# Kernel tuning notes

Measured on AMD Instinct MI355X. Metric: run time of the kernel, lower is better.

The kernel has to match this reference:

```python
import jax, jax.numpy as jnp
import numpy as np

EPS_COMBINE = float(np.finfo(float).eps)  # combined[combined == 0] = np.finfo(float).eps
LOSS_COEF = 0.01


def cv_squared(v):
    # torch .var() is unbiased -> ddof=1
    return jnp.var(v, ddof=1) / (jnp.mean(v) ** 2 + 1e-10)


def setup_inputs() -> dict:
    key = jax.random.key(0)
    k1, k2, k3, k4 = jax.random.split(key, 4)
    B, D, E, C = 4096, 1024, 8, 4096
    x = jax.random.normal(k1, (B, D), jnp.float32)
    # small scale so exp(expert_out) in combine() stays finite
    w_gate = jax.random.normal(k2, (D, E), jnp.float32) * 0.02
    w_exp = jax.random.normal(k3, (E, D, C), jnp.float32) * 0.02
    b_exp = jax.random.normal(k4, (E, C), jnp.float32) * 0.02
    return {"x": x, "w_gate": w_gate, "w_exp": w_exp, "b_exp": b_exp, "k": 4}


def reference(x, w_gate, w_exp, b_exp, k):
    B, D = x.shape
    E = w_gate.shape[1]
    # --- noisy_top_k_gating with noisy_gating=False ---
    logits = x @ w_gate                                   # [B, E]
    top_logits, top_idx = jax.lax.top_k(logits, min(k + 1, E))
    topk_logits = top_logits[:, :k]
    topk_idx = top_idx[:, :k]
    topk_gates = jax.nn.softmax(topk_logits, axis=1)      # softmax over top-k only
    gates = jnp.zeros((B, E), x.dtype).at[jnp.arange(B)[:, None], topk_idx].set(topk_gates)
    importance = gates.sum(0)
    load = (gates > 0).sum(0).astype(jnp.float32)         # _gates_to_load
    loss = (cv_squared(importance) + cv_squared(load)) * LOSS_COEF
    # --- dispatch + per-expert forward + weighted combine ---
    # Experts with gate==0 contribute exactly 0 to the combine, so the dense
    # einsum over all experts computes the same math as SparseDispatcher.
    expert_out = jnp.einsum('bd,edc->bec', x, w_exp) + b_exp   # [B, E, C]
    combined = jnp.einsum('bec,be->bc', jnp.exp(expert_out), gates)  # weighted scatter-combine
    combined = jnp.where(combined == 0, EPS_COMBINE, combined)
    y = jnp.log(combined)
    return y, loss
```

## Files before the change

### kernel.cpp

```cpp
#include <hip/hip_runtime.h>
#include <stdint.h>

#define B_ROWS 4096
#define D_DIM  1024
#define E_NUM  8
#define C_DIM  4096
#define LOSS_COEF 0.01f
#define EPS_COMBINE 2.220446049250313e-16f

typedef float  f32x4  __attribute__((ext_vector_type(4)));
typedef __bf16 bf16x8 __attribute__((ext_vector_type(8)));

static __device__ __forceinline__ unsigned short f2bf(float f) {
    unsigned int u = __float_as_uint(f);
    u += 0x7fffu + ((u >> 16) & 1u);
    return (unsigned short)(u >> 16);
}

static __device__ __forceinline__ void async16(const void* g, void* l) {
    __builtin_amdgcn_global_load_lds(
        (const __attribute__((address_space(1))) unsigned int*)g,
        (__attribute__((address_space(3))) unsigned int*)l, 16, 0, 0);
}

__global__ void zero_stats_kernel(float* __restrict__ stats) {
    if (threadIdx.x < 16) stats[threadIdx.x] = 0.0f;
}

__global__ __launch_bounds__(256) void transpose_wexp_kernel(
    const float* __restrict__ wexp, unsigned short* __restrict__ wT) {
    __shared__ float T[64][68];
    __shared__ unsigned short W[64][72];
    const int e  = blockIdx.z;
    const int k0 = blockIdx.y * 64;
    const int c0 = blockIdx.x * 64;
    const int t  = threadIdx.x;
    const float* src = wexp + ((size_t)e * D_DIM + k0) * C_DIM + c0;
    #pragma unroll
    for (int i = 0; i < 4; ++i) {
        int kr = i * 16 + (t >> 4);
        int cg = (t & 15) * 4;
        *(float4*)&T[kr][cg] = *(const float4*)(src + (size_t)kr * C_DIM + cg);
    }
    __syncthreads();
    {
        const int c  = t & 63;
        const int kq = (t >> 6) * 16;
        unsigned short h[16];
        #pragma unroll
        for (int j = 0; j < 16; ++j) h[j] = f2bf(T[kq + j][c]);
        *(uint4*)&W[c][kq]     = ((const uint4*)h)[0];
        *(uint4*)&W[c][kq + 8] = ((const uint4*)h)[1];
    }
    __syncthreads();
    unsigned short* dstb = wT + (size_t)e * C_DIM * D_DIM;
    #pragma unroll
    for (int r = 0; r < 2; ++r) {
        int i  = r * 256 + t;
        int c3 = i >> 3;
        int k8 = (i & 7) * 8;
        *(uint4*)(dstb + (size_t)(c0 + c3) * D_DIM + k0 + k8) = *(const uint4*)&W[c3][k8];
    }
}

__global__ __launch_bounds__(256) void gating_kernel(
    const float* __restrict__ x,
    const float* __restrict__ wg,
    unsigned short* __restrict__ xb,
    float* __restrict__ gates,
    float* __restrict__ stats) {
    __shared__ float simp[E_NUM], sload[E_NUM];
    const int tid = threadIdx.x;
    if (tid < E_NUM) { simp[tid] = 0.0f; sload[tid] = 0.0f; }
    __syncthreads();
    const int lane = tid & 63;
    const int wid  = tid >> 6;
    const int row  = blockIdx.x * 4 + wid;

    float acc[8] = {0.f,0.f,0.f,0.f,0.f,0.f,0.f,0.f};
    #pragma unroll
    for (int i = 0; i < 4; ++i) {
        int d = i * 256 + lane * 4;
        float4 xv = *(const float4*)(x + (size_t)row * D_DIM + d);
        unsigned short hh[4] = { f2bf(xv.x), f2bf(xv.y), f2bf(xv.z), f2bf(xv.w) };
        *(uint2*)(xb + (size_t)row * D_DIM + d) = *(const uint2*)hh;
        float xa[4] = { xv.x, xv.y, xv.z, xv.w };
        #pragma unroll
        for (int j = 0; j < 4; ++j) {
            const float4* wp = (const float4*)(wg + (size_t)(d + j) * 8);
            float4 w0 = wp[0], w1 = wp[1];
            acc[0] += xa[j] * w0.x; acc[1] += xa[j] * w0.y;
            acc[2] += xa[j] * w0.z; acc[3] += xa[j] * w0.w;
            acc[4] += xa[j] * w1.x; acc[5] += xa[j] * w1.y;
            acc[6] += xa[j] * w1.z; acc[7] += xa[j] * w1.w;
        }
    }
    #pragma unroll
    for (int off = 32; off > 0; off >>= 1)
        #pragma unroll
        for (int e = 0; e < 8; ++e)
            acc[e] += __shfl_xor(acc[e], off, 64);
    if (lane == 0) {
        float val[4]; int idx[4]; unsigned used = 0;
        #pragma unroll
        for (int j = 0; j < 4; ++j) {
            float best = -1e30f; int bi = 0;
            for (int ee = 0; ee < 8; ++ee)
                if (!(used & (1u << ee)) && acc[ee] > best) { best = acc[ee]; bi = ee; }
            used |= 1u << bi; val[j] = best; idx[j] = bi;
        }
        float mx = val[0], sum = 0.f, gv[4];
        #pragma unroll
        for (int j = 0; j < 4; ++j) { gv[j] = __expf(val[j] - mx); sum += gv[j]; }
        float inv = 1.0f / sum;
        float gout[8] = {0.f,0.f,0.f,0.f,0.f,0.f,0.f,0.f};
        #pragma unroll
        for (int j = 0; j < 4; ++j) gout[idx[j]] = gv[j] * inv;
        #pragma unroll
        for (int e = 0; e < 8; ++e) gates[(size_t)row * 8 + e] = gout[e];
        #pragma unroll
        for (int j = 0; j < 4; ++j) {
            atomicAdd(&simp[idx[j]], gv[j] * inv);
            atomicAdd(&sload[idx[j]], 1.0f);
        }
    }
    __syncthreads();
    if (tid < E_NUM) {
        atomicAdd(&stats[tid],          simp[tid]);
        atomicAdd(&stats[E_NUM + tid],  sload[tid]);
    }
}

__global__ void loss_kernel(const float* __restrict__ stats, float* __restrict__ out_loss) {
    if (threadIdx.x == 0) {
        float mi = 0.f, ml = 0.f;
        for (int e = 0; e < 8; ++e) { mi += stats[e]; ml += stats[8 + e]; }
        mi *= 0.125f; ml *= 0.125f;
        float vi = 0.f, vl = 0.f;
        for (int e = 0; e < 8; ++e) {
            float a = stats[e] - mi;     vi += a * a;
            float b = stats[8 + e] - ml; vl += b * b;
        }
        vi *= (1.0f / 7.0f); vl *= (1.0f / 7.0f);
        out_loss[0] = (vi / (mi * mi + 1e-10f) + vl / (ml * ml + 1e-10f)) * LOSS_COEF;
    }
}

__global__ __launch_bounds__(256, 3) void moe_main_kernel(
    const unsigned short* __restrict__ xb,
    const unsigned short* __restrict__ wT,
    const float* __restrict__ bexp,
    const float* __restrict__ gates,
    float* __restrict__ out)
{
    __shared__ unsigned short As[128 * 32];
    __shared__ unsigned short Bs[2 * 64 * 32];
    __shared__ float gs[128 * 9];
    __shared__ float bs[8 * 64];

    const int tid  = threadIdx.x;
    const int lane = tid & 63;
    const int wid  = tid >> 6;
    const int wm   = wid >> 1;
    const int wn   = wid & 1;
    const int q    = lane >> 4;
    const int ln   = lane & 15;
    const int row0 = blockIdx.x * 128;
    const int col0 = blockIdx.y * 64;

    #pragma unroll
    for (int i = 0; i < 4; ++i) {
        int idx = i * 256 + tid;
        gs[(idx >> 3) * 9 + (idx & 7)] = gates[(size_t)row0 * 8 + idx];
    }
    {
        int e = tid >> 5, c = tid & 31;
        bs[e * 64 + c]      = bexp[(size_t)e * C_DIM + col0 + c];
        bs[e * 64 + c + 32] = bexp[(size_t)e * C_DIM + col0 + c + 32];
    }

    const f32x4 vzero = {0.f, 0.f, 0.f, 0.f};
    f32x4 comb[4][2];
    #pragma unroll
    for (int i = 0; i < 4; ++i)
        #pragma unroll
        for (int j = 0; j < 2; ++j) comb[i][j] = vzero;

    const int rS = tid >> 2;
    const int qg = (tid & 3) ^ (rS & 3);
    const unsigned short* gA  = xb + (size_t)(row0 + rS) * D_DIM + qg * 8;
    const unsigned short* gBb = wT + (size_t)(col0 + rS) * D_DIM + qg * 8;
    char* ldsA = (char*)As + wid * 1024;
    char* ldsB = (char*)Bs + wid * 1024;

    const int fq = ((q ^ (ln & 3)) << 3);

    for (int eg = 0; eg < 4; ++eg) {
        f32x4 acc[4][2][2];
        #pragma unroll
        for (int i = 0; i < 4; ++i)
            #pragma unroll
            for (int j = 0; j < 2; ++j)
                #pragma unroll
                for (int e = 0; e < 2; ++e) acc[i][j][e] = vzero;

        const unsigned short* gB0 = gBb + (size_t)(2 * eg)     * C_DIM * D_DIM;
        const unsigned short* gB1 = gBb + (size_t)(2 * eg + 1) * C_DIM * D_DIM;

        for (int kt = 0; kt < D_DIM / 32; ++kt) {
            const int ko = kt * 32;
            async16(gA + ko,               ldsA);
            async16(gA + ko + 64 * D_DIM,  ldsA + 4096);
            async16(gB0 + ko,              ldsB);
            async16(gB1 + ko,              ldsB + 4096);

            __syncthreads();

            bf16x8 af[4], bfr[2][2];
            #pragma unroll
            for (int fm = 0; fm < 4; ++fm)
                af[fm] = *(const bf16x8*)(As + (wm * 64 + fm * 16 + ln) * 32 + fq);
            #pragma unroll
            for (int fn = 0; fn < 2; ++fn)
                #pragma unroll
                for (int e = 0; e < 2; ++e)
                    bfr[fn][e] = *(const bf16x8*)(Bs + e * 2048 +
                                    (wn * 32 + fn * 16 + ln) * 32 + fq);
            #pragma unroll
            for (int fm = 0; fm < 4; ++fm)
                #pragma unroll
                for (int fn = 0; fn < 2; ++fn)
                    #pragma unroll
                    for (int e = 0; e < 2; ++e)
                        acc[fm][fn][e] = __builtin_amdgcn_mfma_f32_16x16x32_bf16(
                            af[fm], bfr[fn][e], acc[fm][fn][e], 0, 0, 0);

            __syncthreads();
        }

        #pragma unroll
        for (int e = 0; e < 2; ++e) {
            int eG = eg * 2 + e;
            #pragma unroll
            for (int fn = 0; fn < 2; ++fn) {
                float bval = bs[eG * 64 + wn * 32 + fn * 16 + ln];
                #pragma unroll
                for (int fm = 0; fm < 4; ++fm)
                    #pragma unroll
                    for (int r = 0; r < 4; ++r) {
                        float g = gs[(wm * 64 + fm * 16 + q * 4 + r) * 9 + eG];
                        comb[fm][fn][r] += g * __expf(acc[fm][fn][e][r] + bval);
                    }
            }
        }
    }

    #pragma unroll
    for (int fm = 0; fm < 4; ++fm)
        #pragma unroll
        for (int fn = 0; fn < 2; ++fn)
            #pragma unroll
            for (int r = 0; r < 4; ++r) {
                int row = row0 + wm * 64 + fm * 16 + q * 4 + r;
                int col = col0 + wn * 32 + fn * 16 + ln;
                float c = comb[fm][fn][r];
                c = (c == 0.0f) ? EPS_COMBINE : c;
                out[(size_t)row * C_DIM + col] = __logf(c);
            }
}

extern "C" void kernel_launch(void* const* d_in, const int* in_sizes, int n_in,
                              void* d_out, int out_size, void* d_ws, size_t ws_size,
                              hipStream_t stream) {
    const float* x    = (const float*)d_in[0];
    const float* wg   = (const float*)d_in[1];
    const float* wexp = (const float*)d_in[2];
    const float* bexp = (const float*)d_in[3];
    float* out = (float*)d_out;
    char*  ws  = (char*)d_ws;

    unsigned short* wT    = (unsigned short*)ws;
    unsigned short* xb    = (unsigned short*)(ws + 67108864);
    float*          gates = (float*)(ws + 75497472);
    float*          stats = (float*)(ws + 75628544);

    zero_stats_kernel<<<1, 64, 0, stream>>>(stats);
    {
        dim3 tg(C_DIM / 64, D_DIM / 64, E_NUM);
        transpose_wexp_kernel<<<tg, 256, 0, stream>>>(wexp, wT);
    }
    gating_kernel<<<B_ROWS / 4, 256, 0, stream>>>(x, wg, xb, gates, stats);
    loss_kernel<<<1, 64, 0, stream>>>(stats, out + (size_t)B_ROWS * C_DIM);

    dim3 grid(B_ROWS / 128, C_DIM / 64);
    moe_main_kernel<<<grid, 256, 0, stream>>>(xb, wT, bexp, gates, out);
}
```

Before: 572.2 us.

## Double-buffer main GEMM LDS loads and merge prep kernels into one launch

```diff
diff --git a/kernel.cpp b/kernel.cpp
--- a/kernel.cpp
+++ b/kernel.cpp
@@ -23,126 +23,111 @@
         (__attribute__((address_space(3))) unsigned int*)l, 16, 0, 0);
 }
 
-__global__ void zero_stats_kernel(float* __restrict__ stats) {
-    if (threadIdx.x < 16) stats[threadIdx.x] = 0.0f;
-}
-
-__global__ __launch_bounds__(256) void transpose_wexp_kernel(
-    const float* __restrict__ wexp, unsigned short* __restrict__ wT) {
-    __shared__ float T[64][68];
-    __shared__ unsigned short W[64][72];
-    const int e  = blockIdx.z;
-    const int k0 = blockIdx.y * 64;
-    const int c0 = blockIdx.x * 64;
-    const int t  = threadIdx.x;
-    const float* src = wexp + ((size_t)e * D_DIM + k0) * C_DIM + c0;
-    #pragma unroll
-    for (int i = 0; i < 4; ++i) {
-        int kr = i * 16 + (t >> 4);
-        int cg = (t & 15) * 4;
-        *(float4*)&T[kr][cg] = *(const float4*)(src + (size_t)kr * C_DIM + cg);
-    }
-    __syncthreads();
-    {
-        const int c  = t & 63;
-        const int kq = (t >> 6) * 16;
-        unsigned short h[16];
-        #pragma unroll
-        for (int j = 0; j < 16; ++j) h[j] = f2bf(T[kq + j][c]);
-        *(uint4*)&W[c][kq]     = ((const uint4*)h)[0];
-        *(uint4*)&W[c][kq + 8] = ((const uint4*)h)[1];
-    }
-    __syncthreads();
-    unsigned short* dstb = wT + (size_t)e * C_DIM * D_DIM;
-    #pragma unroll
-    for (int r = 0; r < 2; ++r) {
-        int i  = r * 256 + t;
-        int c3 = i >> 3;
-        int k8 = (i & 7) * 8;
-        *(uint4*)(dstb + (size_t)(c0 + c3) * D_DIM + k0 + k8) = *(const uint4*)&W[c3][k8];
-    }
-}
-
-__global__ __launch_bounds__(256) void gating_kernel(
+#define NT_BLOCKS ((C_DIM / 64) * (D_DIM / 64) * E_NUM)
+
+__global__ __launch_bounds__(256) void prep_kernel(
     const float* __restrict__ x,
     const float* __restrict__ wg,
+    const float* __restrict__ wexp,
     unsigned short* __restrict__ xb,
+    unsigned short* __restrict__ wT,
     float* __restrict__ gates,
-    float* __restrict__ stats) {
-    __shared__ float simp[E_NUM], sload[E_NUM];
-    const int tid = threadIdx.x;
-    if (tid < E_NUM) { simp[tid] = 0.0f; sload[tid] = 0.0f; }
-    __syncthreads();
-    const int lane = tid & 63;
-    const int wid  = tid >> 6;
-    const int row  = blockIdx.x * 4 + wid;
-
-    float acc[8] = {0.f,0.f,0.f,0.f,0.f,0.f,0.f,0.f};
-    #pragma unroll
-    for (int i = 0; i < 4; ++i) {
-        int d = i * 256 + lane * 4;
-        float4 xv = *(const float4*)(x + (size_t)row * D_DIM + d);
-        unsigned short hh[4] = { f2bf(xv.x), f2bf(xv.y), f2bf(xv.z), f2bf(xv.w) };
-        *(uint2*)(xb + (size_t)row * D_DIM + d) = *(const uint2*)hh;
-        float xa[4] = { xv.x, xv.y, xv.z, xv.w };
-        #pragma unroll
-        for (int j = 0; j < 4; ++j) {
-            const float4* wp = (const float4*)(wg + (size_t)(d + j) * 8);
-            float4 w0 = wp[0], w1 = wp[1];
-            acc[0] += xa[j] * w0.x; acc[1] += xa[j] * w0.y;
-            acc[2] += xa[j] * w0.z; acc[3] += xa[j] * w0.w;
-            acc[4] += xa[j] * w1.x; acc[5] += xa[j] * w1.y;
-            acc[6] += xa[j] * w1.z; acc[7] += xa[j] * w1.w;
-        }
-    }
-    #pragma unroll
-    for (int off = 32; off > 0; off >>= 1)
-        #pragma unroll
-        for (int e = 0; e < 8; ++e)
-            acc[e] += __shfl_xor(acc[e], off, 64);
-    if (lane == 0) {
-        float val[4]; int idx[4]; unsigned used = 0;
-        #pragma unroll
-        for (int j = 0; j < 4; ++j) {
-            float best = -1e30f; int bi = 0;
-            for (int ee = 0; ee < 8; ++ee)
-                if (!(used & (1u << ee)) && acc[ee] > best) { best = acc[ee]; bi = ee; }
-            used |= 1u << bi; val[j] = best; idx[j] = bi;
-        }
-        float mx = val[0], sum = 0.f, gv[4];
-        #pragma unroll
-        for (int j = 0; j < 4; ++j) { gv[j] = __expf(val[j] - mx); sum += gv[j]; }
-        float inv = 1.0f / sum;
-        float gout[8] = {0.f,0.f,0.f,0.f,0.f,0.f,0.f,0.f};
-        #pragma unroll
-        for (int j = 0; j < 4; ++j) gout[idx[j]] = gv[j] * inv;
-        #pragma unroll
-        for (int e = 0; e < 8; ++e) gates[(size_t)row * 8 + e] = gout[e];
-        #pragma unroll
-        for (int j = 0; j < 4; ++j) {
-            atomicAdd(&simp[idx[j]], gv[j] * inv);
-            atomicAdd(&sload[idx[j]], 1.0f);
-        }
-    }
-    __syncthreads();
-    if (tid < E_NUM) {
-        atomicAdd(&stats[tid],          simp[tid]);
-        atomicAdd(&stats[E_NUM + tid],  sload[tid]);
-    }
-}
-
-__global__ void loss_kernel(const float* __restrict__ stats, float* __restrict__ out_loss) {
-    if (threadIdx.x == 0) {
-        float mi = 0.f, ml = 0.f;
-        for (int e = 0; e < 8; ++e) { mi += stats[e]; ml += stats[8 + e]; }
-        mi *= 0.125f; ml *= 0.125f;
-        float vi = 0.f, vl = 0.f;
-        for (int e = 0; e < 8; ++e) {
-            float a = stats[e] - mi;     vi += a * a;
-            float b = stats[8 + e] - ml; vl += b * b;
-        }
-        vi *= (1.0f / 7.0f); vl *= (1.0f / 7.0f);
-        out_loss[0] = (vi / (mi * mi + 1e-10f) + vl / (ml * ml + 1e-10f)) * LOSS_COEF;
+    float* __restrict__ stats)
+{
+    const int t = threadIdx.x;
+    if ((int)blockIdx.x < NT_BLOCKS) {
+        __shared__ float T[64][68];
+        __shared__ unsigned short W[64][72];
+        const int bid = blockIdx.x;
+        const int e  = bid >> 10;
+        const int k0 = ((bid >> 6) & 15) * 64;
+        const int c0 = (bid & 63) * 64;
+        const float* src = wexp + ((size_t)e * D_DIM + k0) * C_DIM + c0;
+        #pragma unroll
+        for (int i = 0; i < 4; ++i) {
+            int kr = i * 16 + (t >> 4);
+            int cg = (t & 15) * 4;
+            *(float4*)&T[kr][cg] = *(const float4*)(src + (size_t)kr * C_DIM + cg);
+        }
+        __syncthreads();
+        {
+            const int c  = t & 63;
+            const int kq = (t >> 6) * 16;
+            unsigned short h[16];
+            #pragma unroll
+            for (int j = 0; j < 16; ++j) h[j] = f2bf(T[kq + j][c]);
+            *(uint4*)&W[c][kq]     = ((const uint4*)h)[0];
+            *(uint4*)&W[c][kq + 8] = ((const uint4*)h)[1];
+        }
+        __syncthreads();
+        unsigned short* dstb = wT + (size_t)e * C_DIM * D_DIM;
+        #pragma unroll
+        for (int r = 0; r < 2; ++r) {
+            int i  = r * 256 + t;
+            int c3 = i >> 3;
+            int k8 = (i & 7) * 8;
+            *(uint4*)(dstb + (size_t)(c0 + c3) * D_DIM + k0 + k8) = *(const uint4*)&W[c3][k8];
+        }
+    } else {
+        __shared__ float simp[E_NUM], sload[E_NUM];
+        if (t < E_NUM) { simp[t] = 0.0f; sload[t] = 0.0f; }
+        __syncthreads();
+        const int lane = t & 63;
+        const int wid  = t >> 6;
+        const int row  = ((int)blockIdx.x - NT_BLOCKS) * 4 + wid;
+
+        float acc[8] = {0.f,0.f,0.f,0.f,0.f,0.f,0.f,0.f};
+        #pragma unroll
+        for (int i = 0; i < 4; ++i) {
+            int d = i * 256 + lane * 4;
+            float4 xv = *(const float4*)(x + (size_t)row * D_DIM + d);
+            unsigned short hh[4] = { f2bf(xv.x), f2bf(xv.y), f2bf(xv.z), f2bf(xv.w) };
+            *(uint2*)(xb + (size_t)row * D_DIM + d) = *(const uint2*)hh;
+            float xa[4] = { xv.x, xv.y, xv.z, xv.w };
+            #pragma unroll
+            for (int j = 0; j < 4; ++j) {
+                const float4* wp = (const float4*)(wg + (size_t)(d + j) * 8);
+                float4 w0 = wp[0], w1 = wp[1];
+                acc[0] += xa[j] * w0.x; acc[1] += xa[j] * w0.y;
+                acc[2] += xa[j] * w0.z; acc[3] += xa[j] * w0.w;
+                acc[4] += xa[j] * w1.x; acc[5] += xa[j] * w1.y;
+                acc[6] += xa[j] * w1.z; acc[7] += xa[j] * w1.w;
+            }
+        }
+        #pragma unroll
+        for (int off = 32; off > 0; off >>= 1)
+            #pragma unroll
+            for (int e = 0; e < 8; ++e)
+                acc[e] += __shfl_xor(acc[e], off, 64);
+        if (lane == 0) {
+            float val[4]; int idx[4]; unsigned used = 0;
+            #pragma unroll
+            for (int j = 0; j < 4; ++j) {
+                float best = -1e30f; int bi = 0;
+                for (int ee = 0; ee < 8; ++ee)
+                    if (!(used & (1u << ee)) && acc[ee] > best) { best = acc[ee]; bi = ee; }
+                used |= 1u << bi; val[j] = best; idx[j] = bi;
+            }
+            float mx = val[0], sum = 0.f, gv[4];
+            #pragma unroll
+            for (int j = 0; j < 4; ++j) { gv[j] = __expf(val[j] - mx); sum += gv[j]; }
+            float inv = 1.0f / sum;
+            float gout[8] = {0.f,0.f,0.f,0.f,0.f,0.f,0.f,0.f};
+            #pragma unroll
+            for (int j = 0; j < 4; ++j) gout[idx[j]] = gv[j] * inv;
+            #pragma unroll
+            for (int e = 0; e < 8; ++e) gates[(size_t)row * 8 + e] = gout[e];
+            #pragma unroll
+            for (int j = 0; j < 4; ++j) {
+                atomicAdd(&simp[idx[j]], gv[j] * inv);
+                atomicAdd(&sload[idx[j]], 1.0f);
+            }
+        }
+        __syncthreads();
+        if (t < E_NUM) {
+            atomicAdd(&stats[t],          simp[t]);
+            atomicAdd(&stats[E_NUM + t],  sload[t]);
+        }
     }
 }
 
@@ -151,10 +136,11 @@
     const unsigned short* __restrict__ wT,
     const float* __restrict__ bexp,
     const float* __restrict__ gates,
+    const float* __restrict__ stats,
     float* __restrict__ out)
 {
-    __shared__ unsigned short As[128 * 32];
-    __shared__ unsigned short Bs[2 * 64 * 32];
+    __shared__ unsigned short As[2][4096];
+    __shared__ unsigned short Bs[2][4096];
     __shared__ float gs[128 * 9];
     __shared__ float bs[8 * 64];
 
@@ -168,6 +154,20 @@
     const int row0 = blockIdx.x * 128;
     const int col0 = blockIdx.y * 64;
 
+    if (blockIdx.x == 0 && blockIdx.y == 0 && tid == 0) {
+        float mi = 0.f, ml = 0.f;
+        for (int e = 0; e < 8; ++e) { mi += stats[e]; ml += stats[8 + e]; }
+        mi *= 0.125f; ml *= 0.125f;
+        float vi = 0.f, vl = 0.f;
+        for (int e = 0; e < 8; ++e) {
+            float a = stats[e] - mi;     vi += a * a;
+            float b = stats[8 + e] - ml; vl += b * b;
+        }
+        vi *= (1.0f / 7.0f); vl *= (1.0f / 7.0f);
+        out[(size_t)B_ROWS * C_DIM] =
+            (vi / (mi * mi + 1e-10f) + vl / (ml * ml + 1e-10f)) * LOSS_COEF;
+    }
+
     #pragma unroll
     for (int i = 0; i < 4; ++i) {
         int idx = i * 256 + tid;
@@ -179,6 +179,25 @@
         bs[e * 64 + c + 32] = bexp[(size_t)e * C_DIM + col0 + c + 32];
     }
 
+    const int sr = tid & 15;
+    const int sq = (tid >> 4) & 3;
+    const unsigned short* gA = xb + (size_t)(row0 + wid * 16 + sr) * D_DIM + sq * 8;
+    const int be = wid >> 1;
+    const unsigned short* gB = wT + (size_t)be * C_DIM * D_DIM
+                             + (size_t)(col0 + (wid & 1) * 32 + sr) * D_DIM + sq * 8;
+
+    char* const a0 = (char*)&As[0][0] + wid * 1024;
+    char* const b0 = (char*)&Bs[0][0] + be * 4096 + (wid & 1) * 2048;
+
+    auto stage = [&](int buf, int eg, int ko) {
+        const size_t bo = (size_t)buf * 8192;
+        async16(gA + ko,              a0 + bo);
+        async16(gA + ko + 64 * D_DIM, a0 + bo + 4096);
+        const unsigned short* gbe = gB + (size_t)eg * 2 * C_DIM * D_DIM + ko;
+        async16(gbe,                  b0 + bo);
+        async16(gbe + 16 * D_DIM,     b0 + bo + 1024);
+    };
+
     const f32x4 vzero = {0.f, 0.f, 0.f, 0.f};
     f32x4 comb[4][2];
     #pragma unroll
@@ -186,14 +205,9 @@
         #pragma unroll
         for (int j = 0; j < 2; ++j) comb[i][j] = vzero;
 
-    const int rS = tid >> 2;
-    const int qg = (tid & 3) ^ (rS & 3);
-    const unsigned short* gA  = xb + (size_t)(row0 + rS) * D_DIM + qg * 8;
-    const unsigned short* gBb = wT + (size_t)(col0 + rS) * D_DIM + qg * 8;
-    char* ldsA = (char*)As + wid * 1024;
-    char* ldsB = (char*)Bs + wid * 1024;
-
-    const int fq = ((q ^ (ln & 3)) << 3);
+    int buf = 0;
+    stage(0, 0, 0);
+    __syncthreads();
 
     for (int eg = 0; eg < 4; ++eg) {
         f32x4 acc[4][2][2];
@@ -204,28 +218,25 @@
                 #pragma unroll
                 for (int e = 0; e < 2; ++e) acc[i][j][e] = vzero;
 
-        const unsigned short* gB0 = gBb + (size_t)(2 * eg)     * C_DIM * D_DIM;
-        const unsigned short* gB1 = gBb + (size_t)(2 * eg + 1) * C_DIM * D_DIM;
-
-        for (int kt = 0; kt < D_DIM / 32; ++kt) {
-            const int ko = kt * 32;
-            async16(gA + ko,               ldsA);
-            async16(gA + ko + 64 * D_DIM,  ldsA + 4096);
-            async16(gB0 + ko,              ldsB);
-            async16(gB1 + ko,              ldsB + 4096);
-
-            __syncthreads();
-
+        for (int kt = 0; kt < 32; ++kt) {
+            const int s = (eg << 5) | kt;
+            if (s < 127) {
+                const int s1 = s + 1;
+                stage(buf ^ 1, s1 >> 5, (s1 & 31) << 5);
+            }
+
+            const unsigned short* pa = &As[buf][0];
+            const unsigned short* pb = &Bs[buf][0];
             bf16x8 af[4], bfr[2][2];
             #pragma unroll
             for (int fm = 0; fm < 4; ++fm)
-                af[fm] = *(const bf16x8*)(As + (wm * 64 + fm * 16 + ln) * 32 + fq);
+                af[fm] = *(const bf16x8*)(pa + (wm * 4 + fm) * 512 + lane * 8);
             #pragma unroll
             for (int fn = 0; fn < 2; ++fn)
                 #pragma unroll
                 for (int e = 0; e < 2; ++e)
-                    bfr[fn][e] = *(const bf16x8*)(Bs + e * 2048 +
-                                    (wn * 32 + fn * 16 + ln) * 32 + fq);
+                    bfr[fn][e] = *(const bf16x8*)(pb + e * 2048 + (wn * 2 + fn) * 512 + lane * 8);
+
             #pragma unroll
             for (int fm = 0; fm < 4; ++fm)
                 #pragma unroll
@@ -236,6 +247,7 @@
                             af[fm], bfr[fn][e], acc[fm][fn][e], 0, 0, 0);
 
             __syncthreads();
+            buf ^= 1;
         }
 
         #pragma unroll
@@ -284,14 +296,10 @@
     float*          gates = (float*)(ws + 75497472);
     float*          stats = (float*)(ws + 75628544);
 
-    zero_stats_kernel<<<1, 64, 0, stream>>>(stats);
-    {
-        dim3 tg(C_DIM / 64, D_DIM / 64, E_NUM);
-        transpose_wexp_kernel<<<tg, 256, 0, stream>>>(wexp, wT);
-    }
-    gating_kernel<<<B_ROWS / 4, 256, 0, stream>>>(x, wg, xb, gates, stats);
-    loss_kernel<<<1, 64, 0, stream>>>(stats, out + (size_t)B_ROWS * C_DIM);
+    hipMemsetAsync(stats, 0, 16 * sizeof(float), stream);
+    prep_kernel<<<NT_BLOCKS + B_ROWS / 4, 256, 0, stream>>>(
+        x, wg, wexp, xb, wT, gates, stats);
 
     dim3 grid(B_ROWS / 128, C_DIM / 64);
-    moe_main_kernel<<<grid, 256, 0, stream>>>(xb, wT, bexp, gates, out);
-}
+    moe_main_kernel<<<grid, 256, 0, stream>>>(xb, wT, bexp, gates, stats, out);
+}
```

Result: slower. 729.2 us (+27.4%).

## Fuse weight transpose and gating into one prep kernel with larger swizzled tiles

Applied to the files above, without the earlier changes.

```diff
diff --git a/kernel.cpp b/kernel.cpp
--- a/kernel.cpp
+++ b/kernel.cpp
@@ -23,111 +23,116 @@
         (__attribute__((address_space(3))) unsigned int*)l, 16, 0, 0);
 }
 
-__global__ void zero_stats_kernel(float* __restrict__ stats) {
-    if (threadIdx.x < 16) stats[threadIdx.x] = 0.0f;
-}
-
-__global__ __launch_bounds__(256) void transpose_wexp_kernel(
-    const float* __restrict__ wexp, unsigned short* __restrict__ wT) {
-    __shared__ float T[64][68];
-    __shared__ unsigned short W[64][72];
-    const int e  = blockIdx.z;
-    const int k0 = blockIdx.y * 64;
-    const int c0 = blockIdx.x * 64;
-    const int t  = threadIdx.x;
-    const float* src = wexp + ((size_t)e * D_DIM + k0) * C_DIM + c0;
-    #pragma unroll
-    for (int i = 0; i < 4; ++i) {
-        int kr = i * 16 + (t >> 4);
-        int cg = (t & 15) * 4;
-        *(float4*)&T[kr][cg] = *(const float4*)(src + (size_t)kr * C_DIM + cg);
-    }
-    __syncthreads();
-    {
-        const int c  = t & 63;
-        const int kq = (t >> 6) * 16;
-        unsigned short h[16];
-        #pragma unroll
-        for (int j = 0; j < 16; ++j) h[j] = f2bf(T[kq + j][c]);
-        *(uint4*)&W[c][kq]     = ((const uint4*)h)[0];
-        *(uint4*)&W[c][kq + 8] = ((const uint4*)h)[1];
-    }
-    __syncthreads();
-    unsigned short* dstb = wT + (size_t)e * C_DIM * D_DIM;
-    #pragma unroll
-    for (int r = 0; r < 2; ++r) {
-        int i  = r * 256 + t;
-        int c3 = i >> 3;
-        int k8 = (i & 7) * 8;
-        *(uint4*)(dstb + (size_t)(c0 + c3) * D_DIM + k0 + k8) = *(const uint4*)&W[c3][k8];
-    }
-}
-
-__global__ __launch_bounds__(256) void gating_kernel(
+#define TP_BLOCKS (8 * 8 * 32)
+
+__global__ __launch_bounds__(256) void prep_kernel(
     const float* __restrict__ x,
     const float* __restrict__ wg,
+    const float* __restrict__ wexp,
     unsigned short* __restrict__ xb,
+    unsigned short* __restrict__ wT,
     float* __restrict__ gates,
-    float* __restrict__ stats) {
-    __shared__ float simp[E_NUM], sload[E_NUM];
-    const int tid = threadIdx.x;
-    if (tid < E_NUM) { simp[tid] = 0.0f; sload[tid] = 0.0f; }
-    __syncthreads();
-    const int lane = tid & 63;
-    const int wid  = tid >> 6;
-    const int row  = blockIdx.x * 4 + wid;
-
-    float acc[8] = {0.f,0.f,0.f,0.f,0.f,0.f,0.f,0.f};
-    #pragma unroll
-    for (int i = 0; i < 4; ++i) {
-        int d = i * 256 + lane * 4;
-        float4 xv = *(const float4*)(x + (size_t)row * D_DIM + d);
-        unsigned short hh[4] = { f2bf(xv.x), f2bf(xv.y), f2bf(xv.z), f2bf(xv.w) };
-        *(uint2*)(xb + (size_t)row * D_DIM + d) = *(const uint2*)hh;
-        float xa[4] = { xv.x, xv.y, xv.z, xv.w };
-        #pragma unroll
-        for (int j = 0; j < 4; ++j) {
-            const float4* wp = (const float4*)(wg + (size_t)(d + j) * 8);
-            float4 w0 = wp[0], w1 = wp[1];
-            acc[0] += xa[j] * w0.x; acc[1] += xa[j] * w0.y;
-            acc[2] += xa[j] * w0.z; acc[3] += xa[j] * w0.w;
-            acc[4] += xa[j] * w1.x; acc[5] += xa[j] * w1.y;
-            acc[6] += xa[j] * w1.z; acc[7] += xa[j] * w1.w;
-        }
-    }
-    #pragma unroll
-    for (int off = 32; off > 0; off >>= 1)
-        #pragma unroll
-        for (int e = 0; e < 8; ++e)
-            acc[e] += __shfl_xor(acc[e], off, 64);
-    if (lane == 0) {
-        float val[4]; int idx[4]; unsigned used = 0;
-        #pragma unroll
-        for (int j = 0; j < 4; ++j) {
-            float best = -1e30f; int bi = 0;
-            for (int ee = 0; ee < 8; ++ee)
-                if (!(used & (1u << ee)) && acc[ee] > best) { best = acc[ee]; bi = ee; }
-            used |= 1u << bi; val[j] = best; idx[j] = bi;
-        }
-        float mx = val[0], sum = 0.f, gv[4];
-        #pragma unroll
-        for (int j = 0; j < 4; ++j) { gv[j] = __expf(val[j] - mx); sum += gv[j]; }
-        float inv = 1.0f / sum;
-        float gout[8] = {0.f,0.f,0.f,0.f,0.f,0.f,0.f,0.f};
-        #pragma unroll
-        for (int j = 0; j < 4; ++j) gout[idx[j]] = gv[j] * inv;
-        #pragma unroll
-        for (int e = 0; e < 8; ++e) gates[(size_t)row * 8 + e] = gout[e];
-        #pragma unroll
-        for (int j = 0; j < 4; ++j) {
-            atomicAdd(&simp[idx[j]], gv[j] * inv);
-            atomicAdd(&sload[idx[j]], 1.0f);
-        }
-    }
-    __syncthreads();
-    if (tid < E_NUM) {
-        atomicAdd(&stats[tid],          simp[tid]);
-        atomicAdd(&stats[E_NUM + tid],  sload[tid]);
+    float* __restrict__ stats)
+{
+    const int t = threadIdx.x;
+    if ((int)blockIdx.x < TP_BLOCKS) {
+        __shared__ unsigned short Tt[128 * 128];
+        const int bid = blockIdx.x;
+        const int ct = bid & 31;
+        const int kt = (bid >> 5) & 7;
+        const int e  = bid >> 8;
+        const int k0 = kt * 128, c0 = ct * 128;
+        const float* src = wexp + ((size_t)e * D_DIM + k0) * C_DIM + c0;
+
+        #pragma unroll
+        for (int i = 0; i < 16; ++i) {
+            const int kr = i * 8 + (t >> 5);
+            const int g  = t & 31;
+            float4 v = *(const float4*)(src + (size_t)kr * C_DIM + g * 4);
+            unsigned short h[4] = { f2bf(v.x), f2bf(v.y), f2bf(v.z), f2bf(v.w) };
+            const int gp = g ^ (((kr >> 4) & 7) << 1);
+            *(uint2*)&Tt[kr * 128 + gp * 4] = *(const uint2*)h;
+        }
+        __syncthreads();
+
+        unsigned short* dst = wT + (size_t)e * C_DIM * D_DIM
+                            + (size_t)c0 * D_DIM + k0;
+        #pragma unroll
+        for (int i = 0; i < 4; ++i) {
+            const int task = i * 256 + t;
+            const int kch  = task & 7;
+            const int c    = task >> 3;
+            const int g    = c >> 2;
+            unsigned short hh[16];
+            #pragma unroll
+            for (int j = 0; j < 16; ++j) {
+                const int k  = kch * 16 + j;
+                const int gp = g ^ (((k >> 4) & 7) << 1);
+                hh[j] = Tt[k * 128 + gp * 4 + (c & 3)];
+            }
+            *(uint4*)(dst + (size_t)c * D_DIM + kch * 16)     = ((const uint4*)hh)[0];
+            *(uint4*)(dst + (size_t)c * D_DIM + kch * 16 + 8) = ((const uint4*)hh)[1];
+        }
+    } else {
+        __shared__ float simp[E_NUM], sload[E_NUM];
+        if (t < E_NUM) { simp[t] = 0.0f; sload[t] = 0.0f; }
+        __syncthreads();
+        const int lane = t & 63;
+        const int wid  = t >> 6;
+        const int row  = ((int)blockIdx.x - TP_BLOCKS) * 4 + wid;
+
+        float acc[8] = {0.f,0.f,0.f,0.f,0.f,0.f,0.f,0.f};
+        #pragma unroll
+        for (int i = 0; i < 4; ++i) {
+            int d = i * 256 + lane * 4;
+            float4 xv = *(const float4*)(x + (size_t)row * D_DIM + d);
+            unsigned short hh[4] = { f2bf(xv.x), f2bf(xv.y), f2bf(xv.z), f2bf(xv.w) };
+            *(uint2*)(xb + (size_t)row * D_DIM + d) = *(const uint2*)hh;
+            float xa[4] = { xv.x, xv.y, xv.z, xv.w };
+            #pragma unroll
+            for (int j = 0; j < 4; ++j) {
+                const float4* wp = (const float4*)(wg + (size_t)(d + j) * 8);
+                float4 w0 = wp[0], w1 = wp[1];
+                acc[0] += xa[j] * w0.x; acc[1] += xa[j] * w0.y;
+                acc[2] += xa[j] * w0.z; acc[3] += xa[j] * w0.w;
+                acc[4] += xa[j] * w1.x; acc[5] += xa[j] * w1.y;
+                acc[6] += xa[j] * w1.z; acc[7] += xa[j] * w1.w;
+            }
+        }
+        #pragma unroll
+        for (int off = 32; off > 0; off >>= 1)
+            #pragma unroll
+            for (int e = 0; e < 8; ++e)
+                acc[e] += __shfl_xor(acc[e], off, 64);
+        if (lane == 0) {
+            float val[4]; int idx[4]; unsigned used = 0;
+            #pragma unroll
+            for (int j = 0; j < 4; ++j) {
+                float best = -1e30f; int bi = 0;
+                for (int ee = 0; ee < 8; ++ee)
+                    if (!(used & (1u << ee)) && acc[ee] > best) { best = acc[ee]; bi = ee; }
+                used |= 1u << bi; val[j] = best; idx[j] = bi;
+            }
+            float mx = val[0], sum = 0.f, gv[4];
+            #pragma unroll
+            for (int j = 0; j < 4; ++j) { gv[j] = __expf(val[j] - mx); sum += gv[j]; }
+            float inv = 1.0f / sum;
+            float gout[8] = {0.f,0.f,0.f,0.f,0.f,0.f,0.f,0.f};
+            #pragma unroll
+            for (int j = 0; j < 4; ++j) gout[idx[j]] = gv[j] * inv;
+            #pragma unroll
+            for (int e = 0; e < 8; ++e) gates[(size_t)row * 8 + e] = gout[e];
+            #pragma unroll
+            for (int j = 0; j < 4; ++j) {
+                atomicAdd(&simp[idx[j]], gv[j] * inv);
+                atomicAdd(&sload[idx[j]], 1.0f);
+            }
+        }
+        __syncthreads();
+        if (t < E_NUM) {
+            atomicAdd(&stats[t],          simp[t]);
+            atomicAdd(&stats[E_NUM + t],  sload[t]);
+        }
     }
 }
 
@@ -179,13 +184,6 @@
         bs[e * 64 + c + 32] = bexp[(size_t)e * C_DIM + col0 + c + 32];
     }
 
-    const f32x4 vzero = {0.f, 0.f, 0.f, 0.f};
-    f32x4 comb[4][2];
-    #pragma unroll
-    for (int i = 0; i < 4; ++i)
-        #pragma unroll
-        for (int j = 0; j < 2; ++j) comb[i][j] = vzero;
-
     const int rS = tid >> 2;
     const int qg = (tid & 3) ^ (rS & 3);
     const unsigned short* gA  = xb + (size_t)(row0 + rS) * D_DIM + qg * 8;
@@ -194,6 +192,13 @@
     char* ldsB = (char*)Bs + wid * 1024;
 
     const int fq = ((q ^ (ln & 3)) << 3);
+
+    const f32x4 vzero = {0.f, 0.f, 0.f, 0.f};
+    f32x4 comb[4][2];
+    #pragma unroll
+    for (int i = 0; i < 4; ++i)
+        #pragma unroll
+        for (int j = 0; j < 2; ++j) comb[i][j] = vzero;
 
     for (int eg = 0; eg < 4; ++eg) {
         f32x4 acc[4][2][2];
@@ -284,12 +289,9 @@
     float*          gates = (float*)(ws + 75497472);
     float*          stats = (float*)(ws + 75628544);
 
-    zero_stats_kernel<<<1, 64, 0, stream>>>(stats);
-    {
-        dim3 tg(C_DIM / 64, D_DIM / 64, E_NUM);
-        transpose_wexp_kernel<<<tg, 256, 0, stream>>>(wexp, wT);
-    }
-    gating_kernel<<<B_ROWS / 4, 256, 0, stream>>>(x, wg, xb, gates, stats);
+    hipMemsetAsync(stats, 0, 16 * sizeof(float), stream);
+    prep_kernel<<<TP_BLOCKS + B_ROWS / 4, 256, 0, stream>>>(
+        x, wg, wexp, xb, wT, gates, stats);
     loss_kernel<<<1, 64, 0, stream>>>(stats, out + (size_t)B_ROWS * C_DIM);
 
     dim3 grid(B_ROWS / 128, C_DIM / 64);
```

Result: faster. 558.8 us (-2.4%).
